# Optimization experiments

Measured on AMD Instinct MI355X. Metric: run time of the kernel, lower is better.

## Reference

```python
import jax, jax.numpy as jnp
import numpy as np

NUM_HEADS = 8


def _layernorm(x, w, b, eps=1e-5):
    # normalize over last axis (channels)
    mu = jnp.mean(x, axis=-1, keepdims=True)
    var = jnp.var(x, axis=-1, keepdims=True)
    return (x - mu) * jax.lax.rsqrt(var + eps) * w + b


def setup_inputs() -> dict:
    key = jax.random.key(0)
    ks = jax.random.split(key, 5)
    B, C, H, W = 8, 512, 32, 32
    x = jax.random.normal(ks[0], (B, C, H, W), dtype=jnp.float32)
    ln_w = jnp.ones((C,), dtype=jnp.float32)
    ln_b = jnp.zeros((C,), dtype=jnp.float32)
    qkv_w = jax.random.normal(ks[1], (3 * C, C), dtype=jnp.float32) * (1.0 / np.sqrt(C))
    qkv_b = jax.random.normal(ks[2], (3 * C,), dtype=jnp.float32) * 0.02
    proj_w = jax.random.normal(ks[3], (C, C), dtype=jnp.float32) * (1.0 / np.sqrt(C))
    proj_b = jax.random.normal(ks[4], (C,), dtype=jnp.float32) * 0.02
    return {"x": x, "ln_w": ln_w, "ln_b": ln_b, "qkv_w": qkv_w,
            "qkv_b": qkv_b, "proj_w": proj_w, "proj_b": proj_b}


def reference(x, ln_w, ln_b, qkv_w, qkv_b, proj_w, proj_b):
    B, C, H, W = x.shape
    nh = NUM_HEADS
    hd = C // nh
    HW = H * W
    residual = x
    # LayerNorm over channels: (B,C,H,W) -> (B,H,W,C)
    xn = _layernorm(x.transpose(0, 2, 3, 1), ln_w, ln_b)  # (B,H,W,C)
    # 1x1 conv == per-pixel linear: (B,H,W,3C)
    qkv = jnp.einsum('bhwc,oc->bhwo', xn, qkv_w) + qkv_b
    # match torch reshape (B,3,nh,hd,HW).permute(1,0,2,4,3)
    qkv = qkv.reshape(B, HW, 3, nh, hd).transpose(2, 0, 3, 1, 4)  # (3,B,nh,HW,hd)
    q, k, v = qkv[0], qkv[1], qkv[2]
    scale = 1.0 / jnp.sqrt(jnp.asarray(hd, dtype=x.dtype))
    attn = jnp.einsum('bnqd,bnkd->bnqk', q, k) * scale  # (B,nh,HW,HW)
    attn = jax.nn.softmax(attn, axis=-1)
    out = jnp.einsum('bnqk,bnkd->bnqd', attn, v)  # (B,nh,HW,hd)
    out = out.transpose(0, 2, 1, 3).reshape(B, H, W, C)
    out = jnp.einsum('bhwc,oc->bhwo', out, proj_w) + proj_b
    return out.transpose(0, 3, 1, 2) + residual
```

## Files before the change

### kernel.cpp

```cpp
#include <hip/hip_runtime.h>

typedef __bf16 bf16;
typedef __bf16 bf16x8 __attribute__((ext_vector_type(8)));
typedef float f32x4 __attribute__((ext_vector_type(4)));
typedef float f32x16 __attribute__((ext_vector_type(16)));

#define MFMA16(a, b, c) __builtin_amdgcn_mfma_f32_16x16x32_bf16(a, b, c, 0, 0, 0)
#define MFMA32(a, b, c) __builtin_amdgcn_mfma_f32_32x32x16_bf16(a, b, c, 0, 0, 0)

#define QSCALE 0.1803368801111137f

static __device__ __forceinline__ unsigned int pack2(float a, float b) {
  unsigned short s0 = __builtin_bit_cast(unsigned short, (bf16)a);
  unsigned short s1 = __builtin_bit_cast(unsigned short, (bf16)b);
  return (unsigned int)s0 | ((unsigned int)s1 << 16);
}

static __device__ __forceinline__ void gl16(const bf16* g, bf16* l) {
  __builtin_amdgcn_global_load_lds(
      (const __attribute__((address_space(1))) unsigned int*)g,
      (__attribute__((address_space(3))) unsigned int*)l, 16, 0, 0);
}

__global__ __launch_bounds__(256) void prep_kernel(
    const float* __restrict__ qkvw, const float* __restrict__ projw,
    bf16* __restrict__ wc, const float* __restrict__ x,
    const float* __restrict__ lnw, const float* __restrict__ lnb,
    bf16* __restrict__ xn) {
  __shared__ float tile[512 * 17];
  __shared__ float wsh[512];
  __shared__ float bsh[512];
  const int t = threadIdx.x;
  if (blockIdx.x < 1024) {
    int c4 = blockIdx.x * 256 + t;
    const float* src = (c4 < 196608) ? (qkvw + (size_t)c4 * 4)
                                     : (projw + (size_t)(c4 - 196608) * 4);
    float4 v = *(const float4*)src;
    uint2 o;
    o.x = pack2(v.x, v.y);
    o.y = pack2(v.z, v.w);
    *(uint2*)&wc[(size_t)c4 * 4] = o;
    return;
  }
  const int bid = blockIdx.x - 1024;
  const int b = bid >> 6;
  const int p0 = (bid & 63) * 16;
  for (int i = t; i < 512; i += 256) {
    wsh[i] = lnw[i];
    bsh[i] = lnb[i];
  }
  const float* xb = x + (size_t)b * 524288 + p0;
#pragma unroll
  for (int i = 0; i < 8; ++i) {
    int chunk = t + 256 * i;
    int c = chunk >> 2, px4 = (chunk & 3) * 4;
    float4 v = *(const float4*)&xb[(size_t)c * 1024 + px4];
    tile[c * 17 + px4 + 0] = v.x;
    tile[c * 17 + px4 + 1] = v.y;
    tile[c * 17 + px4 + 2] = v.z;
    tile[c * 17 + px4 + 3] = v.w;
  }
  __syncthreads();
  const int pix = t >> 4, j = t & 15;
  float sum = 0.f, sq = 0.f;
#pragma unroll
  for (int i = 0; i < 32; ++i) {
    int c = i * 16 + j;
    float v = tile[c * 17 + pix];
    sum += v;
    sq += v * v;
  }
#pragma unroll
  for (int m = 1; m <= 8; m <<= 1) {
    sum += __shfl_xor(sum, m);
    sq += __shfl_xor(sq, m);
  }
  float mu = sum * (1.f / 512.f);
  float var = sq * (1.f / 512.f) - mu * mu;
  float rstd = rsqrtf(var + 1e-5f);
  unsigned int* orow =
      (unsigned int*)(xn + ((size_t)(b * 1024 + p0 + pix)) * 512);
#pragma unroll
  for (int i = 0; i < 16; ++i) {
    int dw = i * 16 + j;
    int c0 = 2 * dw, c1 = 2 * dw + 1;
    float v0 = (tile[c0 * 17 + pix] - mu) * rstd * wsh[c0] + bsh[c0];
    float v1 = (tile[c1 * 17 + pix] - mu) * rstd * wsh[c1] + bsh[c1];
    orow[dw] = pack2(v0, v1);
  }
}

__global__ __launch_bounds__(256, 3) void gemm_qkv(
    const bf16* __restrict__ A, const bf16* __restrict__ Bm,
    const float* __restrict__ bias, bf16* __restrict__ oq,
    bf16* __restrict__ okk, bf16* __restrict__ ov) {
  __shared__ bf16 smem[16384];
  const int t = threadIdx.x;
  const int lane = t & 63, w = t >> 6;
  const int quad = lane >> 4, r16 = lane & 15;
  const int wm = w >> 1, wn = w & 1;
  const int pid = blockIdx.x;
  const int panel = pid / 96, within = pid % 96;
  const int m0 = (panel * 8 + (within & 7)) * 128;
  const int n0 = (within >> 3) * 128;
  int sr[2], sc[2];
#pragma unroll
  for (int j = 0; j < 2; ++j) {
    int c = (w * 2 + j) * 64 + lane;
    int r = c >> 2, g = c & 3;
    sr[j] = r;
    sc[j] = (g ^ ((r >> 1) & 3)) * 8;
  }
  const int gx = (r16 >> 1) & 3;
  f32x4 acc[4][4] = {};
#pragma unroll
  for (int j = 0; j < 2; ++j) {
    gl16(&A[(size_t)(m0 + sr[j]) * 512 + sc[j]], &smem[(w * 2 + j) * 512]);
    gl16(&Bm[(size_t)(n0 + sr[j]) * 512 + sc[j]],
         &smem[8192 + (w * 2 + j) * 512]);
  }
  __syncthreads();
  for (int it = 0; it < 16; ++it) {
    const int cur = it & 1, nxt = cur ^ 1;
    if (it < 15) {
      int k1 = (it + 1) * 32;
#pragma unroll
      for (int j = 0; j < 2; ++j) {
        gl16(&A[(size_t)(m0 + sr[j]) * 512 + k1 + sc[j]],
             &smem[nxt * 4096 + (w * 2 + j) * 512]);
        gl16(&Bm[(size_t)(n0 + sr[j]) * 512 + k1 + sc[j]],
             &smem[8192 + nxt * 4096 + (w * 2 + j) * 512]);
      }
    }
    const bf16* ac = &smem[cur * 4096];
    const bf16* bc = &smem[8192 + cur * 4096];
    bf16x8 af[4], bfr[4];
#pragma unroll
    for (int i = 0; i < 4; ++i) {
      int row = wm * 64 + i * 16 + r16;
      af[i] = *(const bf16x8*)&ac[row * 32 + (quad ^ gx) * 8];
    }
#pragma unroll
    for (int i = 0; i < 4; ++i) {
      int row = wn * 64 + i * 16 + r16;
      bfr[i] = *(const bf16x8*)&bc[row * 32 + (quad ^ gx) * 8];
    }
#pragma unroll
    for (int tm = 0; tm < 4; ++tm)
#pragma unroll
      for (int tn = 0; tn < 4; ++tn)
        acc[tm][tn] = MFMA16(af[tm], bfr[tn], acc[tm][tn]);
    __syncthreads();
  }
  if (n0 < 1024) {
#pragma unroll
    for (int tm = 0; tm < 4; ++tm) {
#pragma unroll
      for (int tn = 0; tn < 4; ++tn) {
        int n = n0 + wn * 64 + tn * 16 + r16;
        float bn = bias[n];
        int comp = n >> 9, h = (n >> 6) & 7, d = n & 63;
#pragma unroll
        for (int r = 0; r < 4; ++r) {
          int m = m0 + wm * 64 + tm * 16 + quad * 4 + r;
          float v = acc[tm][tn][r] + bn;
          int b = m >> 10, p = m & 1023;
          size_t base = ((size_t)(b * 8 + h)) * 65536;
          if (comp == 0)
            oq[base + (size_t)p * 64 + d] = (bf16)(v * QSCALE);
          else
            okk[base + (size_t)p * 64 + d] = (bf16)v;
        }
      }
    }
  } else {
    bf16* tb = &smem[w * 4096];
#pragma unroll
    for (int tn = 0; tn < 4; ++tn) {
      int n = n0 + wn * 64 + tn * 16 + r16;
      float bn = bias[n];
      int row = tn * 16 + r16;
#pragma unroll
      for (int tm = 0; tm < 4; ++tm) {
        f32x4 a = acc[tm][tn];
        uint2 pk;
        pk.x = pack2(a[0] + bn, a[1] + bn);
        pk.y = pack2(a[2] + bn, a[3] + bn);
        int g = (tm * 2 + (quad & 1)) ^ (row & 7);
        *(uint2*)&tb[row * 64 + g * 8 + (quad >> 1) * 4] = pk;
      }
    }
    const int h = ((n0 - 1024) >> 6) + wn;
    const int mw = m0 + wm * 64;
    const int b = mw >> 10;
    bf16* vbase = ov + ((size_t)(b * 8 + h)) * 65536 + (mw & 1023);
#pragma unroll
    for (int pass = 0; pass < 8; ++pass) {
      int row = pass * 8 + (lane >> 3);
      int g = (lane & 7) ^ (row & 7);
      uint4 vd = *(uint4*)&tb[row * 64 + g * 8];
      *(uint4*)&vbase[(size_t)row * 1024 + (lane & 7) * 8] = vd;
    }
  }
}

__global__ __launch_bounds__(256, 4) void gemm_proj(
    const bf16* __restrict__ Wm, const bf16* __restrict__ A,
    const float* __restrict__ bias, const float* __restrict__ resid,
    float* __restrict__ op) {
  __shared__ bf16 ash[2][64 * 64];
  __shared__ bf16 bsh[2][64 * 64];
  const int t = threadIdx.x;
  const int lane = t & 63, w = t >> 6;
  const int quad = lane >> 4, r16 = lane & 15;
  const int wm = w >> 1, wn = w & 1;
  const int m0 = blockIdx.x * 64, n0 = blockIdx.y * 64;
  int soff[2], sr[2];
#pragma unroll
  for (int j = 0; j < 2; ++j) {
    int c = (w * 2 + j) * 64 + lane;
    int r = c >> 3, cc = c & 7;
    sr[j] = r;
    soff[j] = (cc ^ (r & 7)) * 8;
  }
  f32x4 acc[2][2] = {};
#pragma unroll
  for (int j = 0; j < 2; ++j) {
    gl16(&Wm[(size_t)(m0 + sr[j]) * 512 + soff[j]], &ash[0][(w * 2 + j) * 512]);
    gl16(&A[(size_t)(n0 + sr[j]) * 512 + soff[j]], &bsh[0][(w * 2 + j) * 512]);
  }
  __syncthreads();
  for (int it = 0; it < 8; ++it) {
    const int cur = it & 1, nxt = cur ^ 1;
    if (it < 7) {
      int k1 = (it + 1) * 64;
#pragma unroll
      for (int j = 0; j < 2; ++j) {
        gl16(&Wm[(size_t)(m0 + sr[j]) * 512 + k1 + soff[j]],
             &ash[nxt][(w * 2 + j) * 512]);
        gl16(&A[(size_t)(n0 + sr[j]) * 512 + k1 + soff[j]],
             &bsh[nxt][(w * 2 + j) * 512]);
      }
    }
#pragma unroll
    for (int kc = 0; kc < 2; ++kc) {
      bf16x8 af[2], bfr[2];
#pragma unroll
      for (int i = 0; i < 2; ++i) {
        int row = wm * 32 + i * 16 + r16;
        af[i] = *(const bf16x8*)&ash[cur][row * 64 +
                                          ((kc * 4 + quad) ^ (r16 & 7)) * 8];
      }
#pragma unroll
      for (int i = 0; i < 2; ++i) {
        int row = wn * 32 + i * 16 + r16;
        bfr[i] = *(const bf16x8*)&bsh[cur][row * 64 +
                                           ((kc * 4 + quad) ^ (r16 & 7)) * 8];
      }
#pragma unroll
      for (int tm = 0; tm < 2; ++tm)
#pragma unroll
        for (int tn = 0; tn < 2; ++tn)
          acc[tm][tn] = MFMA16(af[tm], bfr[tn], acc[tm][tn]);
    }
    __syncthreads();
  }
#pragma unroll
  for (int tm = 0; tm < 2; ++tm) {
#pragma unroll
    for (int tn = 0; tn < 2; ++tn) {
      int n = n0 + wn * 32 + tn * 16 + r16;
      int b = n >> 10, p = n & 1023;
#pragma unroll
      for (int r = 0; r < 4; ++r) {
        int m = m0 + wm * 32 + tm * 16 + quad * 4 + r;
        size_t idx = ((size_t)(b * 512 + m)) * 1024 + p;
        op[idx] = acc[tm][tn][r] + bias[m] + resid[idx];
      }
    }
  }
}

__global__ __launch_bounds__(256, 1) void attn_kernel(
    const bf16* __restrict__ q, const bf16* __restrict__ k,
    const bf16* __restrict__ vT, bf16* __restrict__ o) {
  __shared__ bf16 kt[2][64 * 64];
  __shared__ bf16 vt[2][64 * 64];
  const int t = threadIdx.x;
  const int lane = t & 63, w = t >> 6;
  const int l31 = lane & 31, hi = lane >> 5;
  const int bh = blockIdx.x;
  const int qt0 = blockIdx.y * 256;
  const bf16* qb = q + (size_t)bh * 65536;
  const bf16* kb = k + (size_t)bh * 65536;
  const bf16* vb = vT + (size_t)bh * 65536;
  const int qra = qt0 + w * 64 + l31;
  bf16x8 qfa[4], qfb[4];
#pragma unroll
  for (int ks = 0; ks < 4; ++ks) {
    qfa[ks] = *(const bf16x8*)&qb[(size_t)qra * 64 + ks * 16 + hi * 8];
    qfb[ks] = *(const bf16x8*)&qb[(size_t)(qra + 32) * 64 + ks * 16 + hi * 8];
  }
  int offk[2], offv[2];
#pragma unroll
  for (int j = 0; j < 2; ++j) {
    int c = (w * 2 + j) * 64 + lane;
    int r = c >> 3, cc = c & 7;
    int sw = (cc ^ (r & 7)) * 8;
    offk[j] = r * 64 + sw;
    offv[j] = r * 1024 + sw;
  }
  f32x16 oacca[2] = {};
  f32x16 oaccb[2] = {};
  float rsa = 0.f, rsb = 0.f;
  const int swz = l31 & 7;
#pragma unroll
  for (int j = 0; j < 2; ++j) {
    gl16(&kb[offk[j]], &kt[0][(w * 2 + j) * 512]);
    gl16(&vb[offv[j]], &vt[0][(w * 2 + j) * 512]);
  }
  __syncthreads();
  for (int it = 0; it < 16; ++it) {
    const int cur = it & 1, nxt = cur ^ 1;
    if (it < 15) {
      int kv1 = (it + 1) * 64;
#pragma unroll
      for (int j = 0; j < 2; ++j) {
        gl16(&kb[(size_t)kv1 * 64 + offk[j]], &kt[nxt][(w * 2 + j) * 512]);
        gl16(&vb[(size_t)kv1 + offv[j]], &vt[nxt][(w * 2 + j) * 512]);
      }
    }
    const bf16* ktc = kt[cur];
    const bf16* vtc = vt[cur];
#pragma unroll
    for (int T = 0; T < 2; ++T) {
      const bf16* kr = &ktc[(T * 32 + l31) * 64];
      f32x16 sa = {}, sb = {};
#pragma unroll
      for (int ks = 0; ks < 4; ++ks) {
        bf16x8 kf = *(const bf16x8*)&kr[((ks * 2 + hi) ^ swz) * 8];
        sa = MFMA32(kf, qfa[ks], sa);
        sb = MFMA32(kf, qfb[ks], sb);
      }
#pragma unroll
      for (int r = 0; r < 16; ++r) {
        float pa = __builtin_exp2f(sa[r]);
        sa[r] = pa;
        rsa += pa;
        float pb = __builtin_exp2f(sb[r]);
        sb[r] = pb;
        rsb += pb;
      }
#pragma unroll
      for (int cc = 0; cc < 2; ++cc) {
        const int c4 = T * 2 + cc, b0 = cc * 8;
        uint4 pua, pub;
        pua.x = pack2(sa[b0 + 0], sa[b0 + 1]);
        pua.y = pack2(sa[b0 + 2], sa[b0 + 3]);
        pua.z = pack2(sa[b0 + 4], sa[b0 + 5]);
        pua.w = pack2(sa[b0 + 6], sa[b0 + 7]);
        pub.x = pack2(sb[b0 + 0], sb[b0 + 1]);
        pub.y = pack2(sb[b0 + 2], sb[b0 + 3]);
        pub.z = pack2(sb[b0 + 4], sb[b0 + 5]);
        pub.w = pack2(sb[b0 + 6], sb[b0 + 7]);
        bf16x8 pfa = __builtin_bit_cast(bf16x8, pua);
        bf16x8 pfb = __builtin_bit_cast(bf16x8, pub);
#pragma unroll
        for (int mf = 0; mf < 2; ++mf) {
          const bf16* vr = &vtc[(mf * 32 + l31) * 64];
          bf16x8 vf = *(const bf16x8*)&vr[((c4 * 2 + hi) ^ swz) * 8];
          oacca[mf] = MFMA32(pfa, vf, oacca[mf]);
          oaccb[mf] = MFMA32(pfb, vf, oaccb[mf]);
        }
      }
    }
    __syncthreads();
  }
  rsa += __shfl_xor(rsa, 32);
  rsb += __shfl_xor(rsb, 32);
  float inva = 1.f / rsa, invb = 1.f / rsb;
  const int b = bh >> 3, h = bh & 7;
#pragma unroll
  for (int r = 0; r < 16; ++r) {
    const int ql = (r & 3) + 8 * (r >> 2) + 4 * hi;
    float iqa = __shfl(inva, ql);
    float iqb = __shfl(invb, ql);
    const int pa = qt0 + w * 64 + ql;
    const size_t ba = ((size_t)(b * 1024 + pa)) * 512 + h * 64;
    const size_t bb = ba + (size_t)32 * 512;
#pragma unroll
    for (int mf = 0; mf < 2; ++mf) {
      o[ba + mf * 32 + l31] = (bf16)(oacca[mf][r] * iqa);
      o[bb + mf * 32 + l31] = (bf16)(oaccb[mf][r] * iqb);
    }
  }
}

extern "C" void kernel_launch(void* const* d_in, const int* in_sizes, int n_in,
                              void* d_out, int out_size, void* d_ws,
                              size_t ws_size, hipStream_t stream) {
  (void)in_sizes;
  (void)n_in;
  (void)out_size;
  (void)ws_size;
  const float* x = (const float*)d_in[0];
  const float* lnw = (const float*)d_in[1];
  const float* lnb = (const float*)d_in[2];
  const float* qkvw = (const float*)d_in[3];
  const float* qkvb = (const float*)d_in[4];
  const float* projw = (const float*)d_in[5];
  const float* projb = (const float*)d_in[6];
  float* out = (float*)d_out;

  const size_t NELEM = 4194304;
  bf16* wc = (bf16*)d_ws;
  bf16* xn = wc + 1048576;
  bf16* qws = xn + NELEM;
  bf16* kws = qws + NELEM;
  bf16* vws = kws + NELEM;
  bf16* aws = xn;

  prep_kernel<<<dim3(1536), dim3(256), 0, stream>>>(qkvw, projw, wc, x, lnw,
                                                    lnb, xn);
  gemm_qkv<<<dim3(768), dim3(256), 0, stream>>>(xn, wc, qkvb, qws, kws, vws);
  attn_kernel<<<dim3(64, 4), dim3(256), 0, stream>>>(qws, kws, vws, aws);
  gemm_proj<<<dim3(8, 128), dim3(256), 0, stream>>>(wc + 786432, aws, projb, x,
                                                    out);
}
```

Measured before the change: 167.1 us.

## Split attention KV range across two wave groups and merge partial sums

After: 157.3 us. 5.9% less time.

```diff
diff --git a/kernel.cpp b/kernel.cpp
--- a/kernel.cpp
+++ b/kernel.cpp
@@ -281,20 +281,21 @@
   }
 }
 
-__global__ __launch_bounds__(256, 1) void attn_kernel(
+__global__ __launch_bounds__(512, 2) void attn_kernel(
     const bf16* __restrict__ q, const bf16* __restrict__ k,
     const bf16* __restrict__ vT, bf16* __restrict__ o) {
-  __shared__ bf16 kt[2][64 * 64];
-  __shared__ bf16 vt[2][64 * 64];
+  __shared__ bf16 smem[32768];
+  __shared__ float rsh[2][4][32];
   const int t = threadIdx.x;
   const int lane = t & 63, w = t >> 6;
+  const int g = w >> 2, wl = w & 3;
   const int l31 = lane & 31, hi = lane >> 5;
   const int bh = blockIdx.x;
   const int qt0 = blockIdx.y * 256;
   const bf16* qb = q + (size_t)bh * 65536;
-  const bf16* kb = k + (size_t)bh * 65536;
-  const bf16* vb = vT + (size_t)bh * 65536;
-  const int qra = qt0 + w * 64 + l31;
+  const bf16* kb = k + (size_t)bh * 65536 + (size_t)g * 32768;
+  const bf16* vb = vT + (size_t)bh * 65536 + (size_t)g * 512;
+  const int qra = qt0 + wl * 64 + l31;
   bf16x8 qfa[4], qfb[4];
 #pragma unroll
   for (int ks = 0; ks < 4; ++ks) {
@@ -304,34 +305,38 @@
   int offk[2], offv[2];
 #pragma unroll
   for (int j = 0; j < 2; ++j) {
-    int c = (w * 2 + j) * 64 + lane;
+    int c = (wl * 2 + j) * 64 + lane;
     int r = c >> 3, cc = c & 7;
     int sw = (cc ^ (r & 7)) * 8;
     offk[j] = r * 64 + sw;
     offv[j] = r * 1024 + sw;
   }
+  bf16* ktg = smem + g * 8192;
+  bf16* vtg = smem + 16384 + g * 8192;
   f32x16 oacca[2] = {};
   f32x16 oaccb[2] = {};
   float rsa = 0.f, rsb = 0.f;
   const int swz = l31 & 7;
 #pragma unroll
   for (int j = 0; j < 2; ++j) {
-    gl16(&kb[offk[j]], &kt[0][(w * 2 + j) * 512]);
-    gl16(&vb[offv[j]], &vt[0][(w * 2 + j) * 512]);
+    gl16(&kb[offk[j]], &ktg[(wl * 2 + j) * 512]);
+    gl16(&vb[offv[j]], &vtg[(wl * 2 + j) * 512]);
   }
   __syncthreads();
-  for (int it = 0; it < 16; ++it) {
+  for (int it = 0; it < 8; ++it) {
     const int cur = it & 1, nxt = cur ^ 1;
-    if (it < 15) {
+    if (it < 7) {
       int kv1 = (it + 1) * 64;
 #pragma unroll
       for (int j = 0; j < 2; ++j) {
-        gl16(&kb[(size_t)kv1 * 64 + offk[j]], &kt[nxt][(w * 2 + j) * 512]);
-        gl16(&vb[(size_t)kv1 + offv[j]], &vt[nxt][(w * 2 + j) * 512]);
-      }
-    }
-    const bf16* ktc = kt[cur];
-    const bf16* vtc = vt[cur];
+        gl16(&kb[(size_t)kv1 * 64 + offk[j]],
+             &ktg[nxt * 4096 + (wl * 2 + j) * 512]);
+        gl16(&vb[(size_t)kv1 + offv[j]],
+             &vtg[nxt * 4096 + (wl * 2 + j) * 512]);
+      }
+    }
+    const bf16* ktc = &ktg[cur * 4096];
+    const bf16* vtc = &vtg[cur * 4096];
 #pragma unroll
     for (int T = 0; T < 2; ++T) {
       const bf16* kr = &ktc[(T * 32 + l31) * 64];
@@ -378,20 +383,42 @@
   }
   rsa += __shfl_xor(rsa, 32);
   rsb += __shfl_xor(rsb, 32);
-  float inva = 1.f / rsa, invb = 1.f / rsb;
-  const int b = bh >> 3, h = bh & 7;
-#pragma unroll
-  for (int r = 0; r < 16; ++r) {
-    const int ql = (r & 3) + 8 * (r >> 2) + 4 * hi;
-    float iqa = __shfl(inva, ql);
-    float iqb = __shfl(invb, ql);
-    const int pa = qt0 + w * 64 + ql;
-    const size_t ba = ((size_t)(b * 1024 + pa)) * 512 + h * 64;
-    const size_t bb = ba + (size_t)32 * 512;
-#pragma unroll
-    for (int mf = 0; mf < 2; ++mf) {
-      o[ba + mf * 32 + l31] = (bf16)(oacca[mf][r] * iqa);
-      o[bb + mf * 32 + l31] = (bf16)(oaccb[mf][r] * iqb);
+  float* cb = (float*)smem;
+  if (g == 1) {
+    float* myb = cb + wl * 4096;
+#pragma unroll
+    for (int mf = 0; mf < 2; ++mf)
+#pragma unroll
+      for (int r = 0; r < 16; ++r) {
+        myb[(mf * 16 + r) * 64 + lane] = oacca[mf][r];
+        myb[(32 + mf * 16 + r) * 64 + lane] = oaccb[mf][r];
+      }
+    if (hi == 0) {
+      rsh[0][wl][l31] = rsa;
+      rsh[1][wl][l31] = rsb;
+    }
+  }
+  __syncthreads();
+  if (g == 0) {
+    const float* pb = cb + wl * 4096;
+    float inva = 1.f / (rsa + rsh[0][wl][l31]);
+    float invb = 1.f / (rsb + rsh[1][wl][l31]);
+    const int b = bh >> 3, h = bh & 7;
+#pragma unroll
+    for (int r = 0; r < 16; ++r) {
+      const int ql = (r & 3) + 8 * (r >> 2) + 4 * hi;
+      float iqa = __shfl(inva, ql);
+      float iqb = __shfl(invb, ql);
+      const int pa = qt0 + wl * 64 + ql;
+      const size_t ba = ((size_t)(b * 1024 + pa)) * 512 + h * 64;
+      const size_t bb = ba + (size_t)32 * 512;
+#pragma unroll
+      for (int mf = 0; mf < 2; ++mf) {
+        float va = oacca[mf][r] + pb[(mf * 16 + r) * 64 + lane];
+        float vb2 = oaccb[mf][r] + pb[(32 + mf * 16 + r) * 64 + lane];
+        o[ba + mf * 32 + l31] = (bf16)(va * iqa);
+        o[bb + mf * 32 + l31] = (bf16)(vb2 * iqb);
+      }
     }
   }
 }
@@ -423,7 +450,7 @@
   prep_kernel<<<dim3(1536), dim3(256), 0, stream>>>(qkvw, projw, wc, x, lnw,
                                                     lnb, xn);
   gemm_qkv<<<dim3(768), dim3(256), 0, stream>>>(xn, wc, qkvb, qws, kws, vws);
-  attn_kernel<<<dim3(64, 4), dim3(256), 0, stream>>>(qws, kws, vws, aws);
+  attn_kernel<<<dim3(64, 4), dim3(512), 0, stream>>>(qws, kws, vws, aws);
   gemm_proj<<<dim3(8, 128), dim3(256), 0, stream>>>(wc + 786432, aws, projb, x,
                                                     out);
 }
```
